# Kernel tuning notes

Measured on AMD Instinct MI355X. Metric: run time of the kernel, lower is better.

## Reference

```python
import jax, jax.numpy as jnp
import numpy as np

N_NODES = 50000
N_EDGES = 800000
NEG_SLOPE = 0.2


def _edge_softmax(scores, dst, n):
    # scores: [E, H]; softmax over edges grouped by destination node
    m = jax.ops.segment_max(scores, dst, num_segments=n)          # [N, H]
    ex = jnp.exp(scores - m[dst])                                 # [E, H]
    s = jax.ops.segment_sum(ex, dst, num_segments=n)              # [N, H]
    return ex / s[dst]


def _gat_layer(h, W, attn_l, attn_r, bias, src, dst, n, heads, out_d):
    feat = (h @ W).reshape(n, heads, out_d)                       # [N, H, D]
    el = jnp.sum(feat * attn_l, axis=-1)                          # [N, H]
    er = jnp.sum(feat * attn_r, axis=-1)                          # [N, H]
    e = jax.nn.leaky_relu(el[src] + er[dst], NEG_SLOPE)           # [E, H]
    alpha = _edge_softmax(e, dst, n)                              # [E, H]
    msg = feat[src] * alpha[:, :, None]                           # [E, H, D]
    rst = jax.ops.segment_sum(msg, dst, num_segments=n)           # [N, H, D]
    return rst + bias.reshape(1, heads, out_d)


def setup_inputs() -> dict:
    key = jax.random.key(0)
    ks = jax.random.split(key, 12)
    in_dim, hid, heads, out_dim = 128, 64, 4, 64
    sc = 0.1
    return {
        "emb": jax.random.normal(ks[0], (N_NODES, in_dim), jnp.float32),
        "src": jax.random.randint(ks[1], (N_EDGES,), 0, N_NODES, jnp.int32),
        "dst": jax.random.randint(ks[2], (N_EDGES,), 0, N_NODES, jnp.int32),
        "W1": jax.random.normal(ks[3], (in_dim, heads * hid), jnp.float32) * sc,
        "attn_l1": jax.random.normal(ks[4], (1, heads, hid), jnp.float32) * sc,
        "attn_r1": jax.random.normal(ks[5], (1, heads, hid), jnp.float32) * sc,
        "b1": jax.random.normal(ks[6], (heads * hid,), jnp.float32) * sc,
        "W2": jax.random.normal(ks[7], (heads * hid, out_dim), jnp.float32) * sc,
        "attn_l2": jax.random.normal(ks[8], (1, 1, out_dim), jnp.float32) * sc,
        "attn_r2": jax.random.normal(ks[9], (1, 1, out_dim), jnp.float32) * sc,
        "b2": jax.random.normal(ks[10], (out_dim,), jnp.float32) * sc,
    }


def reference(emb, src, dst, W1, attn_l1, attn_r1, b1, W2, attn_l2, attn_r2, b2):
    n = emb.shape[0]
    h = _gat_layer(emb, W1, attn_l1, attn_r1, b1, src, dst, n, 4, 64)   # [N,4,64]
    h = jax.nn.relu(h).reshape(n, 4 * 64)                                # [N,256]
    h = _gat_layer(h, W2, attn_l2, attn_r2, b2, src, dst, n, 1, 64)      # [N,1,64]
    return h.reshape(n, 64)
```

## Files before the change

kernel.cpp:

```cpp
#include <hip/hip_runtime.h>
#include <hip/hip_bf16.h>
#include <math.h>

#define DIV_UP(a,b) (((a)+(b)-1)/(b))

typedef __attribute__((ext_vector_type(8))) short short8v;
typedef __attribute__((ext_vector_type(4))) float f32x4;

__device__ __forceinline__ float bf_lo(unsigned u){ union{unsigned x; float f;} v; v.x = u << 16; return v.f; }
__device__ __forceinline__ float bf_hi(unsigned u){ union{unsigned x; float f;} v; v.x = u & 0xffff0000u; return v.f; }
__device__ __forceinline__ unsigned short f2bf(float f){
  union{float f; unsigned u;} v; v.f = f;
  unsigned r = v.u + 0x7fff + ((v.u >> 16) & 1);
  return (unsigned short)(r >> 16);
}
__device__ __forceinline__ unsigned packbf(float a, float b){
  return (unsigned)f2bf(a) | ((unsigned)f2bf(b) << 16);
}
__device__ __forceinline__ float lrelu(float x){ return x > 0.f ? x : 0.2f*x; }

__global__ void k_count_deg(const int* __restrict__ dst, int* __restrict__ deg, int E){
  int i = blockIdx.x*blockDim.x + threadIdx.x;
  if (i < E) atomicAdd(&deg[dst[i]], 1);
}

__global__ __launch_bounds__(256) void k_scan1(const int* __restrict__ deg,
                                               int* __restrict__ blocksum, int N){
  int b = blockIdx.x;
  int base = b*1024 + threadIdx.x*4;
  int s = 0;
  if (base + 3 < N){
    int4 v = *(const int4*)&deg[base];
    s = v.x + v.y + v.z + v.w;
  } else {
    for (int i = 0; i < 4; i++){ int idx = base + i; if (idx < N) s += deg[idx]; }
  }
  #pragma unroll
  for (int o = 32; o; o >>= 1) s += __shfl_down(s, o);
  __shared__ int ws[4];
  int wid = threadIdx.x >> 6, lane = threadIdx.x & 63;
  if (lane == 0) ws[wid] = s;
  __syncthreads();
  if (threadIdx.x == 0) blocksum[b] = ws[0] + ws[1] + ws[2] + ws[3];
}

__global__ __launch_bounds__(256) void k_scan3(const int* __restrict__ deg,
                                               const int* __restrict__ blocksum, int nb,
                                               int* __restrict__ row_start,
                                               int* __restrict__ cursor, int N){
  int b = blockIdx.x;
  __shared__ int s_boff;
  if (threadIdx.x < 64){
    int acc = 0;
    for (int base = 0; base < nb; base += 64){
      int idx = base + threadIdx.x;
      if (idx < nb && idx < b) acc += blocksum[idx];
    }
    #pragma unroll
    for (int o = 32; o; o >>= 1) acc += __shfl_down(acc, o);
    if (threadIdx.x == 0) s_boff = acc;
  }
  int base = b*1024 + threadIdx.x*4;
  int v[4];
  #pragma unroll
  for (int i = 0; i < 4; i++){ int idx = base + i; v[i] = (idx < N) ? deg[idx] : 0; }
  int s = v[0] + v[1] + v[2] + v[3];
  int lane = threadIdx.x & 63, wid = threadIdx.x >> 6;
  int inc = s;
  #pragma unroll
  for (int o = 1; o < 64; o <<= 1){ int t = __shfl_up(inc, o); if (lane >= o) inc += t; }
  __shared__ int wsum[4];
  if (lane == 63) wsum[wid] = inc;
  __syncthreads();
  int woff = 0;
  #pragma unroll
  for (int i = 0; i < 4; i++) if (i < wid) woff += wsum[i];
  int run = s_boff + woff + inc - s;
  #pragma unroll
  for (int i = 0; i < 4; i++){
    int idx = base + i;
    if (idx < N){ row_start[idx] = run; cursor[idx] = run; run += v[i]; }
  }
  if (base < N && base + 4 >= N) row_start[N] = run;
}

__global__ void k_fillw4(const int* __restrict__ dst, const int* __restrict__ src,
                         int* __restrict__ cursor, int* __restrict__ srcp,
                         int* __restrict__ dstp,
                         const float4* __restrict__ el4, const float4* __restrict__ er4,
                         float4* __restrict__ w4, int E){
  int i = blockIdx.x*blockDim.x + threadIdx.x;
  if (i < E){
    int d = dst[i], s = src[i];
    int p = atomicAdd(&cursor[d], 1);
    srcp[p] = s; dstp[p] = d;
    float4 l = el4[s], r = er4[d];
    float4 w;
    w.x = __expf(lrelu(l.x + r.x));
    w.y = __expf(lrelu(l.y + r.y));
    w.z = __expf(lrelu(l.z + r.z));
    w.w = __expf(lrelu(l.w + r.w));
    w4[p] = w;
  }
}

__global__ void k_edgew1(const int* __restrict__ srcp, const int* __restrict__ dstp,
                         const float* __restrict__ el, const float* __restrict__ er,
                         float* __restrict__ w1, int E){
  int i = blockIdx.x*blockDim.x + threadIdx.x;
  if (i < E) w1[i] = __expf(lrelu(el[srcp[i]] + er[dstp[i]]));
}

__global__ __launch_bounds__(256) void k_gemm1loop(const float* __restrict__ A,
      const float* __restrict__ B,
      unsigned short* __restrict__ Cbf,
      const float* __restrict__ al, const float* __restrict__ ar,
      float* __restrict__ el, float* __restrict__ er, int M){
  __shared__ alignas(16) __hip_bfloat16 At[64][136];
  __shared__ alignas(16) __hip_bfloat16 Bt[64][136];
  __shared__ float elp[2][64], erp[2][64];
  const int tid = threadIdx.x;
  const int lane = tid & 63, w = tid >> 6;
  const int mw = w >> 1, nw = w & 1;
  const int m0 = blockIdx.x * 64;
  const int rbase = mw*32, cbase = nw*32;
  const int fr = lane & 15, fg = lane >> 4;

  #pragma unroll
  for (int i = 0; i < 8; i++){
    int q = tid + i*256;
    int row = q >> 5, c4 = q & 31;
    float4 a = make_float4(0.f,0.f,0.f,0.f);
    if (m0 + row < M) a = *(const float4*)&A[(size_t)(m0+row)*128 + c4*4];
    *(uint2*)&At[row][c4*4] = make_uint2(packbf(a.x,a.y), packbf(a.z,a.w));
  }

  for (int by = 0; by < 4; by++){
    int n0 = by * 64;
    __syncthreads();
    #pragma unroll
    for (int i = 0; i < 8; i++){
      int q = tid + i*256;
      int c = q & 63, k4 = q >> 6;
      float b0 = B[(size_t)(k4*4+0)*256 + n0 + c];
      float b1 = B[(size_t)(k4*4+1)*256 + n0 + c];
      float b2 = B[(size_t)(k4*4+2)*256 + n0 + c];
      float b3 = B[(size_t)(k4*4+3)*256 + n0 + c];
      *(uint2*)&Bt[c][k4*4] = make_uint2(packbf(b0,b1), packbf(b2,b3));
    }
    __syncthreads();

    f32x4 acc[2][2];
    #pragma unroll
    for (int i = 0; i < 2; i++)
      #pragma unroll
      for (int jj = 0; jj < 2; jj++)
        #pragma unroll
        for (int r = 0; r < 4; r++) acc[i][jj][r] = 0.f;

    #pragma unroll
    for (int ks = 0; ks < 4; ks++){
      short8v a0 = *(const short8v*)&At[rbase + fr     ][ks*32 + fg*8];
      short8v a1 = *(const short8v*)&At[rbase + 16 + fr][ks*32 + fg*8];
      short8v b0 = *(const short8v*)&Bt[cbase + fr     ][ks*32 + fg*8];
      short8v b1 = *(const short8v*)&Bt[cbase + 16 + fr][ks*32 + fg*8];
      acc[0][0] = __builtin_amdgcn_mfma_f32_16x16x32_bf16(a0, b0, acc[0][0], 0,0,0);
      acc[0][1] = __builtin_amdgcn_mfma_f32_16x16x32_bf16(a0, b1, acc[0][1], 0,0,0);
      acc[1][0] = __builtin_amdgcn_mfma_f32_16x16x32_bf16(a1, b0, acc[1][0], 0,0,0);
      acc[1][1] = __builtin_amdgcn_mfma_f32_16x16x32_bf16(a1, b1, acc[1][1], 0,0,0);
    }

    float alv[2], arv[2];
    #pragma unroll
    for (int nt = 0; nt < 2; nt++){
      int col = cbase + nt*16 + fr;
      alv[nt] = al[n0 + col];
      arv[nt] = ar[n0 + col];
    }
    #pragma unroll
    for (int mt = 0; mt < 2; mt++){
      #pragma unroll
      for (int r = 0; r < 4; r++){
        float pl = acc[mt][0][r]*alv[0] + acc[mt][1][r]*alv[1];
        float pr = acc[mt][0][r]*arv[0] + acc[mt][1][r]*arv[1];
        #pragma unroll
        for (int o = 1; o < 16; o <<= 1){ pl += __shfl_xor(pl, o); pr += __shfl_xor(pr, o); }
        if (fr == 0){
          int rl = rbase + mt*16 + fg*4 + r;
          elp[nw][rl] = pl; erp[nw][rl] = pr;
        }
      }
    }
    #pragma unroll
    for (int mt = 0; mt < 2; mt++){
      #pragma unroll
      for (int r = 0; r < 4; r++){
        int row = m0 + rbase + mt*16 + fg*4 + r;
        if (row < M){
          #pragma unroll
          for (int nt = 0; nt < 2; nt++)
            Cbf[(size_t)row*256 + n0 + cbase + nt*16 + fr] = f2bf(acc[mt][nt][r]);
        }
      }
    }
    __syncthreads();
    if (tid < 64){
      int row = m0 + tid;
      if (row < M){
        el[(size_t)row*4 + by] = elp[0][tid] + elp[1][tid];
        er[(size_t)row*4 + by] = erp[0][tid] + erp[1][tid];
      }
    }
  }
}

template<int K, int H, bool ABF>
__global__ __launch_bounds__(256) void k_gemm_mfma(const void* __restrict__ Av,
      const float* __restrict__ B, int ldb,
      unsigned short* __restrict__ Cbf,
      const float* __restrict__ al, const float* __restrict__ ar,
      float* __restrict__ el, float* __restrict__ er, int M){
  constexpr int KP = K + 8;
  __shared__ alignas(16) __hip_bfloat16 At[64][KP];
  __shared__ alignas(16) __hip_bfloat16 Bt[64][KP];
  __shared__ float elp[2][64], erp[2][64];
  const int tid = threadIdx.x;
  const int lane = tid & 63, w = tid >> 6;
  const int mw = w >> 1, nw = w & 1;
  const int m0 = blockIdx.x * 64, by = blockIdx.y, n0 = by * 64;

  if constexpr (!ABF){
    const float* A = (const float*)Av;
    #pragma unroll
    for (int i = 0; i < K/16; i++){
      int q = tid + i*256;
      int row = q / (K/4), c4 = q % (K/4);
      float4 a = make_float4(0.f,0.f,0.f,0.f);
      if (m0 + row < M) a = *(const float4*)&A[(size_t)(m0+row)*K + c4*4];
      *(uint2*)&At[row][c4*4] = make_uint2(packbf(a.x,a.y), packbf(a.z,a.w));
    }
  } else {
    const __hip_bfloat16* A = (const __hip_bfloat16*)Av;
    #pragma unroll
    for (int i = 0; i < K/32; i++){
      int q = tid + i*256;
      int row = q / (K/8), c8 = q % (K/8);
      uint4 u = make_uint4(0,0,0,0);
      if (m0 + row < M) u = *(const uint4*)&A[(size_t)(m0+row)*K + c8*8];
      *(uint4*)&At[row][c8*8] = u;
    }
  }
  #pragma unroll
  for (int i = 0; i < K/16; i++){
    int q = tid + i*256;
    int c = q & 63, k4 = q >> 6;
    float b0 = B[(size_t)(k4*4+0)*ldb + n0 + c];
    float b1 = B[(size_t)(k4*4+1)*ldb + n0 + c];
    float b2 = B[(size_t)(k4*4+2)*ldb + n0 + c];
    float b3 = B[(size_t)(k4*4+3)*ldb + n0 + c];
    *(uint2*)&Bt[c][k4*4] = make_uint2(packbf(b0,b1), packbf(b2,b3));
  }
  __syncthreads();

  f32x4 acc[2][2];
  #pragma unroll
  for (int i = 0; i < 2; i++)
    #pragma unroll
    for (int j = 0; j < 2; j++)
      #pragma unroll
      for (int r = 0; r < 4; r++) acc[i][j][r] = 0.f;

  const int rbase = mw*32, cbase = nw*32;
  const int fr = lane & 15, fg = lane >> 4;
  #pragma unroll
  for (int ks = 0; ks < K/32; ks++){
    short8v a0 = *(const short8v*)&At[rbase + fr     ][ks*32 + fg*8];
    short8v a1 = *(const short8v*)&At[rbase + 16 + fr][ks*32 + fg*8];
    short8v b0 = *(const short8v*)&Bt[cbase + fr     ][ks*32 + fg*8];
    short8v b1 = *(const short8v*)&Bt[cbase + 16 + fr][ks*32 + fg*8];
    acc[0][0] = __builtin_amdgcn_mfma_f32_16x16x32_bf16(a0, b0, acc[0][0], 0,0,0);
    acc[0][1] = __builtin_amdgcn_mfma_f32_16x16x32_bf16(a0, b1, acc[0][1], 0,0,0);
    acc[1][0] = __builtin_amdgcn_mfma_f32_16x16x32_bf16(a1, b0, acc[1][0], 0,0,0);
    acc[1][1] = __builtin_amdgcn_mfma_f32_16x16x32_bf16(a1, b1, acc[1][1], 0,0,0);
  }

  float alv[2], arv[2];
  #pragma unroll
  for (int nt = 0; nt < 2; nt++){
    int col = cbase + nt*16 + fr;
    alv[nt] = al[by*64 + col];
    arv[nt] = ar[by*64 + col];
  }
  #pragma unroll
  for (int mt = 0; mt < 2; mt++){
    #pragma unroll
    for (int r = 0; r < 4; r++){
      float pl = acc[mt][0][r]*alv[0] + acc[mt][1][r]*alv[1];
      float pr = acc[mt][0][r]*arv[0] + acc[mt][1][r]*arv[1];
      #pragma unroll
      for (int o = 1; o < 16; o <<= 1){ pl += __shfl_xor(pl, o); pr += __shfl_xor(pr, o); }
      if (fr == 0){
        int rl = rbase + mt*16 + fg*4 + r;
        elp[nw][rl] = pl; erp[nw][rl] = pr;
      }
    }
  }
  const int NN = H*64;
  #pragma unroll
  for (int mt = 0; mt < 2; mt++){
    #pragma unroll
    for (int r = 0; r < 4; r++){
      int row = m0 + rbase + mt*16 + fg*4 + r;
      if (row < M){
        #pragma unroll
        for (int nt = 0; nt < 2; nt++)
          Cbf[(size_t)row*NN + n0 + cbase + nt*16 + fr] = f2bf(acc[mt][nt][r]);
      }
    }
  }
  __syncthreads();
  if (tid < 64){
    int row = m0 + tid;
    if (row < M){
      el[(size_t)row*H + by] = elp[0][tid] + elp[1][tid];
      er[(size_t)row*H + by] = erp[0][tid] + erp[1][tid];
    }
  }
}

__global__ __launch_bounds__(256) void k_gath4(const uint4* __restrict__ fbase,
      const float* __restrict__ w4, const int* __restrict__ row_start,
      const int* __restrict__ srcp, const float* __restrict__ bias,
      __hip_bfloat16* __restrict__ outb, int N, int nwaves){
  int wv = threadIdx.x >> 6, lane = threadIdx.x & 63;
  int g = lane >> 4, j = lane & 15, h = j >> 2;
  const unsigned jo2 = (unsigned)(j << 1);

  int n = blockIdx.x*4 + wv;
  if (n >= N) return;
  int rs = row_start[n], re = row_start[n+1];

  while (true){
    int deg = re - rs;
    int nn = n + nwaves;
    int rs_n = 0, re_n = 0;
    if (nn < N){ rs_n = row_start[nn]; re_n = row_start[nn+1]; }

    float acc[16];
    #pragma unroll
    for (int k = 0; k < 16; k++) acc[k] = 0.f;
    float Sacc = 0.f;

    int i = 0;
    int full = deg & ~15;
    for (; i < full; i += 16){
      float wb[4]; uint4 u0[4], u1[4];
      #pragma unroll
      for (int k = 0; k < 4; k++){
        unsigned e = (unsigned)(rs + i + k*4 + g);
        int sb = srcp[e];
        wb[k] = w4[(e << 2) + h];
        unsigned fi = ((unsigned)sb << 5) + jo2;
        u0[k] = fbase[fi];
        u1[k] = fbase[fi + 1];
      }
      #pragma unroll
      for (int k = 0; k < 4; k++){
        float wk = wb[k];
        Sacc += wk;
        acc[0]  += bf_lo(u0[k].x)*wk; acc[1]  += bf_hi(u0[k].x)*wk;
        acc[2]  += bf_lo(u0[k].y)*wk; acc[3]  += bf_hi(u0[k].y)*wk;
        acc[4]  += bf_lo(u0[k].z)*wk; acc[5]  += bf_hi(u0[k].z)*wk;
        acc[6]  += bf_lo(u0[k].w)*wk; acc[7]  += bf_hi(u0[k].w)*wk;
        acc[8]  += bf_lo(u1[k].x)*wk; acc[9]  += bf_hi(u1[k].x)*wk;
        acc[10] += bf_lo(u1[k].y)*wk; acc[11] += bf_hi(u1[k].y)*wk;
        acc[12] += bf_lo(u1[k].z)*wk; acc[13] += bf_hi(u1[k].z)*wk;
        acc[14] += bf_lo(u1[k].w)*wk; acc[15] += bf_hi(u1[k].w)*wk;
      }
    }
    if (i < deg){
      float wb[4]; uint4 u0[4], u1[4];
      #pragma unroll
      for (int k = 0; k < 4; k++){
        int e = i + k*4 + g;
        wb[k] = 0.f;
        u0[k] = make_uint4(0,0,0,0); u1[k] = make_uint4(0,0,0,0);
        if (e < deg){
          unsigned ee = (unsigned)(rs + e);
          int sb = srcp[ee];
          wb[k] = w4[(ee << 2) + h];
          unsigned fi = ((unsigned)sb << 5) + jo2;
          u0[k] = fbase[fi];
          u1[k] = fbase[fi + 1];
        }
      }
      #pragma unroll
      for (int k = 0; k < 4; k++){
        float wk = wb[k];
        Sacc += wk;
        acc[0]  += bf_lo(u0[k].x)*wk; acc[1]  += bf_hi(u0[k].x)*wk;
        acc[2]  += bf_lo(u0[k].y)*wk; acc[3]  += bf_hi(u0[k].y)*wk;
        acc[4]  += bf_lo(u0[k].z)*wk; acc[5]  += bf_hi(u0[k].z)*wk;
        acc[6]  += bf_lo(u0[k].w)*wk; acc[7]  += bf_hi(u0[k].w)*wk;
        acc[8]  += bf_lo(u1[k].x)*wk; acc[9]  += bf_hi(u1[k].x)*wk;
        acc[10] += bf_lo(u1[k].y)*wk; acc[11] += bf_hi(u1[k].y)*wk;
        acc[12] += bf_lo(u1[k].z)*wk; acc[13] += bf_hi(u1[k].z)*wk;
        acc[14] += bf_lo(u1[k].w)*wk; acc[15] += bf_hi(u1[k].w)*wk;
      }
    }

    #pragma unroll
    for (int k = 0; k < 16; k++){
      acc[k] += __shfl_xor(acc[k], 16);
      acc[k] += __shfl_xor(acc[k], 32);
    }
    Sacc += __shfl_xor(Sacc, 16);
    Sacc += __shfl_xor(Sacc, 32);
    if (g == 0){
      float inv = (deg > 0 && Sacc > 0.f) ? 1.f / Sacc : 0.f;
      float4 b0 = *(const float4*)&bias[j*16 + 0];
      float4 b1 = *(const float4*)&bias[j*16 + 4];
      float4 b2 = *(const float4*)&bias[j*16 + 8];
      float4 b3 = *(const float4*)&bias[j*16 + 12];
      float v[16];
      v[0]=acc[0]*inv+b0.x;  v[1]=acc[1]*inv+b0.y;  v[2]=acc[2]*inv+b0.z;  v[3]=acc[3]*inv+b0.w;
      v[4]=acc[4]*inv+b1.x;  v[5]=acc[5]*inv+b1.y;  v[6]=acc[6]*inv+b1.z;  v[7]=acc[7]*inv+b1.w;
      v[8]=acc[8]*inv+b2.x;  v[9]=acc[9]*inv+b2.y;  v[10]=acc[10]*inv+b2.z; v[11]=acc[11]*inv+b2.w;
      v[12]=acc[12]*inv+b3.x; v[13]=acc[13]*inv+b3.y; v[14]=acc[14]*inv+b3.z; v[15]=acc[15]*inv+b3.w;
      #pragma unroll
      for (int k = 0; k < 16; k++) v[k] = fmaxf(v[k], 0.f);
      uint4 o0, o1;
      o0.x = packbf(v[0], v[1]);   o0.y = packbf(v[2], v[3]);
      o0.z = packbf(v[4], v[5]);   o0.w = packbf(v[6], v[7]);
      o1.x = packbf(v[8], v[9]);   o1.y = packbf(v[10], v[11]);
      o1.z = packbf(v[12], v[13]); o1.w = packbf(v[14], v[15]);
      uint4* op = (uint4*)outb + (size_t)n*32 + (j << 1);
      op[0] = o0; op[1] = o1;
    }

    if (nn >= N) break;
    n = nn; rs = rs_n; re = re_n;
  }
}

__global__ __launch_bounds__(256) void k_gath1(const uint2* __restrict__ fbase,
      const float* __restrict__ w1, const int* __restrict__ row_start,
      const int* __restrict__ srcp, const float* __restrict__ bias,
      float* __restrict__ out, int N, int nwaves){
  int wv = threadIdx.x >> 6, lane = threadIdx.x & 63;
  int g = lane >> 4, j = lane & 15;
  const unsigned jo = (unsigned)j;

  int n = blockIdx.x*4 + wv;
  if (n >= N) return;
  int rs = row_start[n], re = row_start[n+1];

  while (true){
    int deg = re - rs;
    int nn = n + nwaves;
    int rs_n = 0, re_n = 0;
    if (nn < N){ rs_n = row_start[nn]; re_n = row_start[nn+1]; }

    float acc[4] = {0.f, 0.f, 0.f, 0.f};
    float Sacc = 0.f;

    int i = 0;
    int full = deg & ~15;
    for (; i < full; i += 16){
      float wb[4]; uint2 u[4];
      #pragma unroll
      for (int k = 0; k < 4; k++){
        unsigned e = (unsigned)(rs + i + k*4 + g);
        int sb = srcp[e];
        wb[k] = w1[e];
        u[k] = fbase[((unsigned)sb << 4) + jo];
      }
      #pragma unroll
      for (int k = 0; k < 4; k++){
        float wk = wb[k];
        Sacc += wk;
        acc[0] += bf_lo(u[k].x)*wk; acc[1] += bf_hi(u[k].x)*wk;
        acc[2] += bf_lo(u[k].y)*wk; acc[3] += bf_hi(u[k].y)*wk;
      }
    }
    if (i < deg){
      float wb[4]; uint2 u[4];
      #pragma unroll
      for (int k = 0; k < 4; k++){
        int e = i + k*4 + g;
        wb[k] = 0.f;
        u[k] = make_uint2(0,0);
        if (e < deg){
          unsigned ee = (unsigned)(rs + e);
          int sb = srcp[ee];
          wb[k] = w1[ee];
          u[k] = fbase[((unsigned)sb << 4) + jo];
        }
      }
      #pragma unroll
      for (int k = 0; k < 4; k++){
        float wk = wb[k];
        Sacc += wk;
        acc[0] += bf_lo(u[k].x)*wk; acc[1] += bf_hi(u[k].x)*wk;
        acc[2] += bf_lo(u[k].y)*wk; acc[3] += bf_hi(u[k].y)*wk;
      }
    }

    #pragma unroll
    for (int k = 0; k < 4; k++){
      acc[k] += __shfl_xor(acc[k], 16);
      acc[k] += __shfl_xor(acc[k], 32);
    }
    Sacc += __shfl_xor(Sacc, 16);
    Sacc += __shfl_xor(Sacc, 32);
    if (g == 0){
      float inv = (deg > 0 && Sacc > 0.f) ? 1.f / Sacc : 0.f;
      float4 b = *(const float4*)&bias[j*4];
      float4 o;
      o.x = acc[0]*inv + b.x; o.y = acc[1]*inv + b.y;
      o.z = acc[2]*inv + b.z; o.w = acc[3]*inv + b.w;
      *(float4*)&out[(size_t)n*64 + j*4] = o;
    }

    if (nn >= N) break;
    n = nn; rs = rs_n; re = re_n;
  }
}

extern "C" void kernel_launch(void* const* d_in, const int* in_sizes, int n_in,
                              void* d_out, int out_size, void* d_ws, size_t ws_size,
                              hipStream_t stream) {
  const float* emb = (const float*)d_in[0];
  const int*   src = (const int*)d_in[1];
  const int*   dst = (const int*)d_in[2];
  const float* W1  = (const float*)d_in[3];
  const float* al1 = (const float*)d_in[4];
  const float* ar1 = (const float*)d_in[5];
  const float* b1  = (const float*)d_in[6];
  const float* W2  = (const float*)d_in[7];
  const float* al2 = (const float*)d_in[8];
  const float* ar2 = (const float*)d_in[9];
  const float* b2  = (const float*)d_in[10];
  float* out = (float*)d_out;

  const int N = in_sizes[0] / 128;
  const int E = in_sizes[1];

  char* p = (char*)d_ws;
  auto alloc = [&](size_t bytes) -> void* {
    void* r = (void*)p; p += (bytes + 255) & ~(size_t)255; return r;
  };
  __hip_bfloat16* feat1b = (__hip_bfloat16*)alloc((size_t)N*256*2);
  __hip_bfloat16* h1b    = (__hip_bfloat16*)alloc((size_t)N*256*2);
  __hip_bfloat16* feat2b = (__hip_bfloat16*)alloc((size_t)N*64*2);
  float* el1             = (float*)alloc((size_t)N*4*4);
  float* er1             = (float*)alloc((size_t)N*4*4);
  float* el2             = (float*)alloc((size_t)N*4);
  float* er2             = (float*)alloc((size_t)N*4);
  int*   deg             = (int*)alloc((size_t)N*4);
  int*   row_start       = (int*)alloc((size_t)(N+1)*4);
  int*   cursor          = (int*)alloc((size_t)N*4);
  int*   blocksum        = (int*)alloc((size_t)DIV_UP(N,1024)*4);
  int*   srcp            = (int*)alloc((size_t)E*4);
  int*   dstp            = (int*)alloc((size_t)E*4);
  float* w4              = (float*)alloc((size_t)E*16);
  float* w1              = w4;

  const int nb = DIV_UP(N, 1024);
  const int gblocks = min(DIV_UP(N, 4), 2048);
  const int nwaves  = gblocks * 4;

  hipMemsetAsync(deg, 0, (size_t)N*4, stream);
  k_count_deg<<<DIV_UP(E,256), 256, 0, stream>>>(dst, deg, E);
  k_scan1<<<nb, 256, 0, stream>>>(deg, blocksum, N);
  k_scan3<<<nb, 256, 0, stream>>>(deg, blocksum, nb, row_start, cursor, N);

  k_gemm1loop<<<DIV_UP(N,64), 256, 0, stream>>>(emb, W1, (unsigned short*)feat1b,
                                                al1, ar1, el1, er1, N);
  k_fillw4<<<DIV_UP(E,256), 256, 0, stream>>>(dst, src, cursor, srcp, dstp,
      (const float4*)el1, (const float4*)er1, (float4*)w4, E);
  k_gath4<<<gblocks, 256, 0, stream>>>((const uint4*)feat1b, w4, row_start,
                                       srcp, b1, h1b, N, nwaves);
  k_gemm_mfma<256,1,true><<<dim3(DIV_UP(N,64), 1), 256, 0, stream>>>(
      h1b, W2, 64, (unsigned short*)feat2b, al2, ar2, el2, er2, N);
  k_edgew1<<<DIV_UP(E,256), 256, 0, stream>>>(srcp, dstp, el2, er2, w1, E);
  k_gath1<<<gblocks, 256, 0, stream>>>((const uint2*)feat2b, w1, row_start,
                                       srcp, b2, out, N, nwaves);
}
```

Before: 229.3 us.

## Fuse degree counting into GEMM1 launch and compute layer-2 edge weights in gather

```diff
diff --git a/kernel.cpp b/kernel.cpp
--- a/kernel.cpp
+++ b/kernel.cpp
@@ -18,11 +18,6 @@
   return (unsigned)f2bf(a) | ((unsigned)f2bf(b) << 16);
 }
 __device__ __forceinline__ float lrelu(float x){ return x > 0.f ? x : 0.2f*x; }
-
-__global__ void k_count_deg(const int* __restrict__ dst, int* __restrict__ deg, int E){
-  int i = blockIdx.x*blockDim.x + threadIdx.x;
-  if (i < E) atomicAdd(&deg[dst[i]], 1);
-}
 
 __global__ __launch_bounds__(256) void k_scan1(const int* __restrict__ deg,
                                                int* __restrict__ blocksum, int N){
@@ -86,14 +81,13 @@
 
 __global__ void k_fillw4(const int* __restrict__ dst, const int* __restrict__ src,
                          int* __restrict__ cursor, int* __restrict__ srcp,
-                         int* __restrict__ dstp,
                          const float4* __restrict__ el4, const float4* __restrict__ er4,
                          float4* __restrict__ w4, int E){
   int i = blockIdx.x*blockDim.x + threadIdx.x;
   if (i < E){
     int d = dst[i], s = src[i];
     int p = atomicAdd(&cursor[d], 1);
-    srcp[p] = s; dstp[p] = d;
+    srcp[p] = s;
     float4 l = el4[s], r = er4[d];
     float4 w;
     w.x = __expf(lrelu(l.x + r.x));
@@ -104,21 +98,22 @@
   }
 }
 
-__global__ void k_edgew1(const int* __restrict__ srcp, const int* __restrict__ dstp,
-                         const float* __restrict__ el, const float* __restrict__ er,
-                         float* __restrict__ w1, int E){
-  int i = blockIdx.x*blockDim.x + threadIdx.x;
-  if (i < E) w1[i] = __expf(lrelu(el[srcp[i]] + er[dstp[i]]));
-}
-
-__global__ __launch_bounds__(256) void k_gemm1loop(const float* __restrict__ A,
+__global__ __launch_bounds__(256) void k_gemm1_count(const float* __restrict__ A,
       const float* __restrict__ B,
       unsigned short* __restrict__ Cbf,
       const float* __restrict__ al, const float* __restrict__ ar,
-      float* __restrict__ el, float* __restrict__ er, int M){
+      float* __restrict__ el, float* __restrict__ er, int M,
+      const int* __restrict__ dst, int* __restrict__ deg, int E, int gemmBlocks){
   __shared__ alignas(16) __hip_bfloat16 At[64][136];
   __shared__ alignas(16) __hip_bfloat16 Bt[64][136];
   __shared__ float elp[2][64], erp[2][64];
+
+  if (blockIdx.x >= gemmBlocks){
+    int i = (blockIdx.x - gemmBlocks)*256 + threadIdx.x;
+    if (i < E) atomicAdd(&deg[dst[i]], 1);
+    return;
+  }
+
   const int tid = threadIdx.x;
   const int lane = tid & 63, w = tid >> 6;
   const int mw = w >> 1, nw = w & 1;
@@ -444,9 +439,9 @@
 }
 
 __global__ __launch_bounds__(256) void k_gath1(const uint2* __restrict__ fbase,
-      const float* __restrict__ w1, const int* __restrict__ row_start,
-      const int* __restrict__ srcp, const float* __restrict__ bias,
-      float* __restrict__ out, int N, int nwaves){
+      const float* __restrict__ el2, const float* __restrict__ er2,
+      const int* __restrict__ row_start, const int* __restrict__ srcp,
+      const float* __restrict__ bias, float* __restrict__ out, int N, int nwaves){
   int wv = threadIdx.x >> 6, lane = threadIdx.x & 63;
   int g = lane >> 4, j = lane & 15;
   const unsigned jo = (unsigned)j;
@@ -461,6 +456,7 @@
     int rs_n = 0, re_n = 0;
     if (nn < N){ rs_n = row_start[nn]; re_n = row_start[nn+1]; }
 
+    float ern = er2[n];
     float acc[4] = {0.f, 0.f, 0.f, 0.f};
     float Sacc = 0.f;
 
@@ -472,7 +468,9 @@
       for (int k = 0; k < 4; k++){
         unsigned e = (unsigned)(rs + i + k*4 + g);
         int sb = srcp[e];
-        wb[k] = w1[e];
+        float x = el2[sb] + ern;
+        x = x > 0.f ? x : 0.2f*x;
+        wb[k] = __expf(x);
         u[k] = fbase[((unsigned)sb << 4) + jo];
       }
       #pragma unroll
@@ -493,7 +491,9 @@
         if (e < deg){
           unsigned ee = (unsigned)(rs + e);
           int sb = srcp[ee];
-          wb[k] = w1[ee];
+          float x = el2[sb] + ern;
+          x = x > 0.f ? x : 0.2f*x;
+          wb[k] = __expf(x);
           u[k] = fbase[((unsigned)sb << 4) + jo];
         }
       }
@@ -562,28 +562,29 @@
   int*   cursor          = (int*)alloc((size_t)N*4);
   int*   blocksum        = (int*)alloc((size_t)DIV_UP(N,1024)*4);
   int*   srcp            = (int*)alloc((size_t)E*4);
-  int*   dstp            = (int*)alloc((size_t)E*4);
   float* w4              = (float*)alloc((size_t)E*16);
-  float* w1              = w4;
 
   const int nb = DIV_UP(N, 1024);
   const int gblocks = min(DIV_UP(N, 4), 2048);
   const int nwaves  = gblocks * 4;
+  const int gemmBlocks = DIV_UP(N, 64);
+  const int cntBlocks  = DIV_UP(E, 256);
 
   hipMemsetAsync(deg, 0, (size_t)N*4, stream);
-  k_count_deg<<<DIV_UP(E,256), 256, 0, stream>>>(dst, deg, E);
+
+  k_gemm1_count<<<gemmBlocks + cntBlocks, 256, 0, stream>>>(
+      emb, W1, (unsigned short*)feat1b, al1, ar1, el1, er1, N,
+      dst, deg, E, gemmBlocks);
+
   k_scan1<<<nb, 256, 0, stream>>>(deg, blocksum, N);
   k_scan3<<<nb, 256, 0, stream>>>(deg, blocksum, nb, row_start, cursor, N);
-
-  k_gemm1loop<<<DIV_UP(N,64), 256, 0, stream>>>(emb, W1, (unsigned short*)feat1b,
-                                                al1, ar1, el1, er1, N);
-  k_fillw4<<<DIV_UP(E,256), 256, 0, stream>>>(dst, src, cursor, srcp, dstp,
+  k_fillw4<<<DIV_UP(E,256), 256, 0, stream>>>(dst, src, cursor, srcp,
       (const float4*)el1, (const float4*)er1, (float4*)w4, E);
+
   k_gath4<<<gblocks, 256, 0, stream>>>((const uint4*)feat1b, w4, row_start,
                                        srcp, b1, h1b, N, nwaves);
   k_gemm_mfma<256,1,true><<<dim3(DIV_UP(N,64), 1), 256, 0, stream>>>(
       h1b, W2, 64, (unsigned short*)feat2b, al2, ar2, el2, er2, N);
-  k_edgew1<<<DIV_UP(E,256), 256, 0, stream>>>(srcp, dstp, el2, er2, w1, E);
-  k_gath1<<<gblocks, 256, 0, stream>>>((const uint2*)feat2b, w1, row_start,
-                                       srcp, b2, out, N, nwaves);
-}
+  k_gath1<<<gblocks, 256, 0, stream>>>((const uint2*)feat2b, el2, er2,
+                                       row_start, srcp, b2, out, N, nwaves);
+}
```

After: 200.0 us, median of 2. 1.15x faster.
